# Kernel optimization log

Hardware: AMD Instinct MI355X
Metric: run time of the kernel (lower is better)

Reference implementation:

```python
import jax, jax.numpy as jnp
import numpy as np

N_NODES = 40962
LATENT_DIM = 512
N_EDGES = 655392
NUM_BLOCKS = 4
NUM_HEADS = 4
NUM_FREQ = 32
BASE_PERIOD = 16
NOISE_EMB_DIM = 16
EPS = 1e-5


def setup_inputs() -> dict:
    key = jax.random.key(0)
    ks = jax.random.split(key, 20)
    def w(k, shape, s=0.02):
        return jax.random.normal(k, shape, dtype=jnp.float32) * s
    D, B, C = LATENT_DIM, NUM_BLOCKS, NOISE_EMB_DIM
    z = lambda *s: jnp.zeros(s, jnp.float32)
    return {
        'latent_mesh_nodes': jax.random.normal(ks[0], (N_NODES, D), dtype=jnp.float32),
        'edge_index': jax.random.randint(ks[1], (2, N_EDGES), 0, N_NODES, dtype=jnp.int32),
        'noise_levels': jax.random.uniform(ks[2], (N_NODES, 1), dtype=jnp.float32),
        # Fourier embedding MLP (2F -> C -> C, SiLU)
        'f_w1': w(ks[3], (2 * NUM_FREQ, C)), 'f_b1': z(C),
        'f_w2': w(ks[4], (C, C)), 'f_b2': z(C),
        # per-block conditional LayerNorm 1 (FiLM)
        's1_w': w(ks[5], (B, C, D)), 's1_b': z(B, D),
        'b1_w': w(ks[6], (B, C, D)), 'b1_b': z(B, D),
        # per-block sparse MHA projections
        'wq': w(ks[7], (B, D, D)), 'bq': z(B, D),
        'wk': w(ks[8], (B, D, D)), 'bk': z(B, D),
        'wv': w(ks[9], (B, D, D)), 'bv': z(B, D),
        'wo': w(ks[10], (B, D, D)), 'bo': z(B, D),
        # per-block conditional LayerNorm 2 (FiLM)
        's2_w': w(ks[11], (B, C, D)), 's2_b': z(B, D),
        'b2_w': w(ks[12], (B, C, D)), 'b2_b': z(B, D),
        # per-block feed-forward MLP (D -> D -> D, ReLU)
        'm_w1': w(ks[13], (B, D, D)), 'm_b1': z(B, D),
        'm_w2': w(ks[14], (B, D, D)), 'm_b2': z(B, D),
    }


def _cond_layer_norm(x, cond, sw, sb, bw, bb):
    # LayerNorm without affine params, then FiLM from noise embedding.
    mu = jnp.mean(x, axis=-1, keepdims=True)
    var = jnp.var(x, axis=-1, keepdims=True)
    xn = (x - mu) * jax.lax.rsqrt(var + EPS)
    scale = cond @ sw + sb  # (N, D)
    bias = cond @ bw + bb
    return xn * (1.0 + scale) + bias


def _sparse_attention(x, src, dst, wq, bq, wk, bk, wv, bv, wo, bo):
    N, D = x.shape
    H, Dh = NUM_HEADS, D // NUM_HEADS
    q = ((x @ wq + bq)).reshape(N, H, Dh) * (Dh ** -0.5)
    k = (x @ wk + bk).reshape(N, H, Dh)
    v = (x @ wv + bv).reshape(N, H, Dh)
    # per-edge scores: row (query) = src, col (key) = dst, per head
    scores = jnp.einsum('ehd,ehd->eh', q[src], k[dst])  # (E, H)
    smax = jax.ops.segment_max(scores, src, num_segments=N)  # (N, H)
    ex = jnp.exp(scores - smax[src])
    denom = jax.ops.segment_sum(ex, src, num_segments=N)
    attn = ex / denom[src]  # row-wise sparse softmax
    out = jax.ops.segment_sum(attn[:, :, None] * v[dst], src, num_segments=N)
    return out.reshape(N, D) @ wo + bo


def _forward(x, edge_index, noise_levels, f_w1, f_b1, f_w2, f_b2,
             s1_w, s1_b, b1_w, b1_b, wq, bq, wk, bk, wv, bv, wo, bo,
             s2_w, s2_b, b2_w, b2_b, m_w1, m_b1, m_w2, m_b2):
    src, dst = edge_index[0], edge_index[1]
    # Fourier noise embedding
    freqs = jnp.arange(1, NUM_FREQ + 1, dtype=x.dtype) * (2.0 * np.pi / BASE_PERIOD)
    ph = noise_levels * freqs  # (N, F)
    emb = jnp.concatenate([jnp.sin(ph), jnp.cos(ph)], axis=-1)
    cond = jax.nn.silu(emb @ f_w1 + f_b1) @ f_w2 + f_b2  # (N, C)
    for i in range(NUM_BLOCKS):
        y = _cond_layer_norm(x, cond, s1_w[i], s1_b[i], b1_w[i], b1_b[i])
        y = _sparse_attention(y, src, dst, wq[i], bq[i], wk[i], bk[i],
                              wv[i], bv[i], wo[i], bo[i])
        x = x + y
        y = _cond_layer_norm(x, cond, s2_w[i], s2_b[i], b2_w[i], b2_b[i])
        y = jax.nn.relu(y @ m_w1[i] + m_b1[i]) @ m_w2[i] + m_b2[i]
        x = x + y
    return x


def reference(latent_mesh_nodes, edge_index, noise_levels, f_w1, f_b1, f_w2, f_b2,
              s1_w, s1_b, b1_w, b1_b, wq, bq, wk, bk, wv, bv, wo, bo,
              s2_w, s2_b, b2_w, b2_b, m_w1, m_b1, m_w2, m_b2):
    return _forward(latent_mesh_nodes, edge_index, noise_levels, f_w1, f_b1, f_w2, f_b2,
                    s1_w, s1_b, b1_w, b1_b, wq, bq, wk, bk, wv, bv, wo, bo,
                    s2_w, s2_b, b2_w, b2_b, m_w1, m_b1, m_w2, m_b2)
```

## Files before the change

kernel.cpp:

```cpp
#include <hip/hip_runtime.h>
#include <hip/hip_bf16.h>
#include <stdint.h>

#define N_NODES 40962
#define LATENT  512
#define N_EDGES 655392
#define NFREQ   32
#define NOISE_C 16

typedef unsigned short u16;
typedef unsigned char u8;
typedef __attribute__((ext_vector_type(8))) short short8;
typedef __attribute__((ext_vector_type(4))) float f32x4;
typedef __attribute__((ext_vector_type(2))) float f32x2;

__device__ __forceinline__ float bf2f(u16 u) {
  return __uint_as_float(((uint32_t)u) << 16);
}
__device__ __forceinline__ u16 f2bf(float f) {
  uint32_t u = __float_as_uint(f);
  u += 0x7fffu + ((u >> 16) & 1u);
  return (u16)(u >> 16);
}

__device__ __forceinline__ u8 f2fp8(float f) {
#if __has_builtin(__builtin_amdgcn_cvt_pk_fp8_f32)
  int pk = __builtin_amdgcn_cvt_pk_fp8_f32(f, f, 0, false);
  return (u8)(pk & 0xff);
#else
  uint32_t x = __float_as_uint(f);
  uint32_t s = (x >> 24) & 0x80;
  uint32_t y = x & 0x7fffffff;
  if (__uint_as_float(y) >= 448.f) return (u8)(s | 0x7e);
  y += 0xfffff + ((y >> 20) & 1);
  int e = (int)(y >> 23) - 127 + 7;
  uint32_t m = (y >> 20) & 7;
  if (e < 1) return (u8)s;
  if (e > 15 || (e == 15 && m == 7)) return (u8)(s | 0x7e);
  return (u8)(s | ((uint32_t)e << 3) | m);
#endif
}

__device__ __forceinline__ void fp8x4_to_f32(uint32_t w, float* o) {
#if __has_builtin(__builtin_amdgcn_cvt_pk_f32_fp8)
  f32x2 lo = __builtin_amdgcn_cvt_pk_f32_fp8(w, false);
  f32x2 hi = __builtin_amdgcn_cvt_pk_f32_fp8(w, true);
  o[0] = lo.x; o[1] = lo.y; o[2] = hi.x; o[3] = hi.y;
#else
  #pragma unroll
  for (int i = 0; i < 4; ++i) {
    uint32_t u = (w >> (8 * i)) & 0xff;
    uint32_t e = (u >> 3) & 15, m = u & 7, s = (u & 0x80) << 24;
    o[i] = (e == 0) ? __uint_as_float(s)
                    : __uint_as_float(s | ((e + 120) << 23) | (m << 20));
  }
#endif
}

__global__ void cond_kernel(const float* __restrict__ noise,
                            const float* __restrict__ w1, const float* __restrict__ b1,
                            const float* __restrict__ w2, const float* __restrict__ b2,
                            float* __restrict__ cond)
{
  int n = blockIdx.x * blockDim.x + threadIdx.x;
  if (n >= N_NODES) return;
  float nv = noise[n];
  float emb[2 * NFREQ];
  #pragma unroll
  for (int f = 0; f < NFREQ; ++f) {
    float ph = nv * (0.39269908169872414f * (float)(f + 1));
    emb[f] = __sinf(ph);
    emb[NFREQ + f] = __cosf(ph);
  }
  float h[NOISE_C];
  #pragma unroll
  for (int c = 0; c < NOISE_C; ++c) {
    float a = b1[c];
    for (int j = 0; j < 2 * NFREQ; ++j) a = fmaf(emb[j], w1[j * NOISE_C + c], a);
    h[c] = a * (1.f / (1.f + __expf(-a)));
  }
  #pragma unroll
  for (int c2 = 0; c2 < NOISE_C; ++c2) {
    float a = b2[c2];
    #pragma unroll
    for (int c = 0; c < NOISE_C; ++c) a = fmaf(h[c], w2[c * NOISE_C + c2], a);
    cond[(size_t)n * NOISE_C + c2] = a;
  }
}

__global__ void conv_weights(const float* __restrict__ wq, const float* __restrict__ wk,
                             const float* __restrict__ wv, const float* __restrict__ wo,
                             const float* __restrict__ m1, const float* __restrict__ m2,
                             u16* __restrict__ out)
{
  __shared__ float tile[32][33];
  int z = blockIdx.z;
  int t6 = z >> 2;
  const float* W = (t6 == 0) ? wq : (t6 == 1) ? wk : (t6 == 2) ? wv :
                   (t6 == 3) ? wo : (t6 == 4) ? m1 : m2;
  W += (size_t)(z & 3) * 262144;
  u16* O = out + (size_t)((z & 3) * 6 + t6) * 262144;
  int tx = threadIdx.x, ty = threadIdx.y;
  int j0 = blockIdx.x * 32, k0 = blockIdx.y * 32;
  #pragma unroll
  for (int r = ty; r < 32; r += 8)
    tile[r][tx] = W[(size_t)(k0 + r) * 512 + j0 + tx];
  __syncthreads();
  #pragma unroll
  for (int r = ty; r < 32; r += 8)
    O[(size_t)(j0 + r) * 512 + k0 + tx] = f2bf(tile[tx][r]);
}

__global__ void pack_bias(const float* __restrict__ bq, const float* __restrict__ bk,
                          const float* __restrict__ bv, float* __restrict__ bqkv)
{
  int idx = blockIdx.x * 256 + threadIdx.x;
  if (idx >= 4 * 1536) return;
  int i = idx / 1536, c = idx % 1536;
  float v = (c < 512) ? bq[i * 512 + c] : (c < 1024) ? bk[i * 512 + c - 512]
                                                     : bv[i * 512 + c - 1024];
  bqkv[idx] = v;
}

__global__ void hist_kernel(const int* __restrict__ src, int* __restrict__ deg) {
  int e = blockIdx.x * 256 + threadIdx.x;
  if (e < N_EDGES) atomicAdd(&deg[src[e]], 1);
}

__global__ __launch_bounds__(1024) void scan_kernel(const int* __restrict__ deg,
                                                    int* __restrict__ row_start)
{
  __shared__ int sums[1024];
  int t = threadIdx.x;
  const int chunk = (N_NODES + 1023) / 1024;
  int lo = t * chunk, hi = lo + chunk;
  if (lo > N_NODES) lo = N_NODES;
  if (hi > N_NODES) hi = N_NODES;
  int s = 0;
  for (int i = lo; i < hi; ++i) s += deg[i];
  sums[t] = s;
  __syncthreads();
  for (int off = 1; off < 1024; off <<= 1) {
    int v = (t >= off) ? sums[t - off] : 0;
    __syncthreads();
    sums[t] += v;
    __syncthreads();
  }
  int base = (t > 0) ? sums[t - 1] : 0;
  for (int i = lo; i < hi; ++i) { row_start[i] = base; base += deg[i]; }
  if (t == 1023) row_start[N_NODES] = sums[1023];
}

__global__ void scatter_kernel(const int* __restrict__ src, const int* __restrict__ dst,
                               const int* __restrict__ row_start, int* __restrict__ cursor,
                               int* __restrict__ csr_dst)
{
  int e = blockIdx.x * 256 + threadIdx.x;
  if (e >= N_EDGES) return;
  int s = src[e];
  int p = atomicAdd(&cursor[s], 1);
  csr_dst[row_start[s] + p] = dst[e];
}

__global__ __launch_bounds__(256) void ln_film(
  const float* __restrict__ x, const float* __restrict__ cond,
  const float* __restrict__ sw, const float* __restrict__ sb,
  const float* __restrict__ bw, const float* __restrict__ bb,
  u16* __restrict__ yb)
{
  int n = blockIdx.x;
  int t = threadIdx.x;
  const float* xr = x + (size_t)n * 512;
  float v0 = xr[t], v1 = xr[t + 256];
  float s = v0 + v1, ss = v0 * v0 + v1 * v1;
  #pragma unroll
  for (int o = 32; o > 0; o >>= 1) { s += __shfl_down(s, o); ss += __shfl_down(ss, o); }
  __shared__ float red[8];
  __shared__ float cl[16];
  int wv_ = t >> 6, ln_ = t & 63;
  if (ln_ == 0) { red[wv_] = s; red[4 + wv_] = ss; }
  if (t < 16) cl[t] = cond[(size_t)n * 16 + t];
  __syncthreads();
  s  = red[0] + red[1] + red[2] + red[3];
  ss = red[4] + red[5] + red[6] + red[7];
  float mu = s * (1.f / 512.f);
  float rstd = rsqrtf(ss * (1.f / 512.f) - mu * mu + 1e-5f);
  #pragma unroll
  for (int k = 0; k < 2; ++k) {
    int d = t + k * 256;
    float sc = sb[d], bi = bb[d];
    #pragma unroll
    for (int c = 0; c < 16; ++c) {
      sc = fmaf(cl[c], sw[c * 512 + d], sc);
      bi = fmaf(cl[c], bw[c * 512 + d], bi);
    }
    float xv = k ? v1 : v0;
    yb[(size_t)n * 512 + d] = f2bf((xv - mu) * rstd * (1.f + sc) + bi);
  }
}

template<int MODE, bool RELU, bool RES>
__global__ __launch_bounds__(256) void gemm_bt(
  const u16* __restrict__ A, const u16* __restrict__ Bt,
  const float* __restrict__ bias, const float* __restrict__ res,
  float* __restrict__ Cf, u16* __restrict__ Cb, u8* __restrict__ Cq)
{
  constexpr int M = N_NODES, K = 512;
  __shared__ u16 As[2 * 128 * 32];
  __shared__ u16 Bs[2 * 128 * 32];
  int tid = threadIdx.x;
  int wave = tid >> 6, lane = tid & 63;
  int tn = blockIdx.x * 128, tm = blockIdx.y * 128;
  f32x4 acc[4][4] = {};
  int wm = (wave & 1) * 64, wn = (wave >> 1) * 64;
  int fm = lane & 15, fq = lane >> 4;

  auto stage = [&](int buf, int k0) {
    #pragma unroll
    for (int rr = 0; rr < 2; ++rr) {
      int c = rr * 256 + tid;
      int row = c >> 2, cb = (c & 3) << 3;
      int gr = tm + row; if (gr > M - 1) gr = M - 1;
      __builtin_amdgcn_global_load_lds(
        (const __attribute__((address_space(1))) void*)(uintptr_t)(A + (size_t)gr * K + (k0 + cb)),
        (__attribute__((address_space(3))) void*)(uintptr_t)(As + buf * 4096 + (size_t)(rr * 256 + wave * 64) * 8),
        16, 0, 0);
      int brow = tn + row;
      __builtin_amdgcn_global_load_lds(
        (const __attribute__((address_space(1))) void*)(uintptr_t)(Bt + (size_t)brow * K + (k0 + cb)),
        (__attribute__((address_space(3))) void*)(uintptr_t)(Bs + buf * 4096 + (size_t)(rr * 256 + wave * 64) * 8),
        16, 0, 0);
    }
  };

  stage(0, 0);
  #pragma unroll 4
  for (int it = 0; it < K / 32; ++it) {
    int cur = it & 1;
    __syncthreads();
    if (it + 1 < K / 32) stage(cur ^ 1, (it + 1) * 32);
    const u16* Ab = As + cur * 4096;
    const u16* Bb = Bs + cur * 4096;
    short8 af[4], bf_[4];
    #pragma unroll
    for (int i = 0; i < 4; ++i) {
      af[i]  = *(const short8*)(Ab + (wm + i * 16 + fm) * 32 + fq * 8);
      bf_[i] = *(const short8*)(Bb + (wn + i * 16 + fm) * 32 + fq * 8);
    }
    #pragma unroll
    for (int mi = 0; mi < 4; ++mi)
      #pragma unroll
      for (int ni = 0; ni < 4; ++ni)
        acc[mi][ni] = __builtin_amdgcn_mfma_f32_16x16x32_bf16(af[mi], bf_[ni], acc[mi][ni], 0, 0, 0);
  }

  #pragma unroll
  for (int mi = 0; mi < 4; ++mi) {
    #pragma unroll
    for (int ni = 0; ni < 4; ++ni) {
      int col = tn + wn + ni * 16 + fm;
      float bvv = bias[col];
      int rowb = tm + wm + mi * 16 + fq * 4;
      #pragma unroll
      for (int r = 0; r < 4; ++r) {
        int gr = rowb + r;
        if (gr < M) {
          float v = acc[mi][ni][r] + bvv;
          if (RELU) v = fmaxf(v, 0.f);
          if (RES)  v += res[(size_t)gr * 512 + col];
          if (MODE == 0) {
            Cf[(size_t)gr * 512 + col] = v;
          } else if (MODE == 1) {
            Cb[(size_t)gr * 512 + col] = f2bf(v);
          } else {
            u8* row_p = Cq + (size_t)gr * 2048;
            if (col < 512) *(u16*)(row_p + 2 * col) = f2bf(v);
            else           row_p[512 + col] = f2fp8(v);
          }
        }
      }
    }
  }
}

__global__ __launch_bounds__(256) void attn_kernel(
  const u8* __restrict__ qkv,
  const int* __restrict__ row_start, const int* __restrict__ csr_dst,
  u16* __restrict__ ab)
{
  int wave = threadIdx.x >> 6, lane = threadIdx.x & 63;
  int n = blockIdx.x * 4 + wave;
  if (n >= N_NODES) return;
  float qf[8];
  {
    short8 q8 = *(const short8*)(qkv + (size_t)n * 2048 + lane * 16);
    #pragma unroll
    for (int j = 0; j < 8; ++j) qf[j] = bf2f((u16)q8[j]);
  }
  float m = -1e30f, l = 0.f;
  float acc[8];
  #pragma unroll
  for (int j = 0; j < 8; ++j) acc[j] = 0.f;
  int e0 = row_start[n], e1 = row_start[n + 1];
  int deg = e1 - e0;
  if (deg > 0) {
    int koff = 1024 + lane * 8, voff = 1536 + lane * 8;
    int d0 = csr_dst[e0];
    int d1 = (deg > 1) ? csr_dst[e0 + 1] : d0;
    uint2 ku0 = *(const uint2*)(qkv + (size_t)d0 * 2048 + koff);
    uint2 vu0 = *(const uint2*)(qkv + (size_t)d0 * 2048 + voff);
    uint2 ku1 = *(const uint2*)(qkv + (size_t)d1 * 2048 + koff);
    uint2 vu1 = *(const uint2*)(qkv + (size_t)d1 * 2048 + voff);
    for (int t = 0; t < deg; t += 2) {
      int p0 = e0 + t + 2, p1 = e0 + t + 3;
      int dn0 = (p0 < e1) ? csr_dst[p0] : d0;
      int dn1 = (p1 < e1) ? csr_dst[p1] : d0;
      uint2 kn0 = *(const uint2*)(qkv + (size_t)dn0 * 2048 + koff);
      uint2 vn0 = *(const uint2*)(qkv + (size_t)dn0 * 2048 + voff);
      uint2 kn1 = *(const uint2*)(qkv + (size_t)dn1 * 2048 + koff);
      uint2 vn1 = *(const uint2*)(qkv + (size_t)dn1 * 2048 + voff);
      float k0f[8], k1f[8];
      fp8x4_to_f32(ku0.x, k0f); fp8x4_to_f32(ku0.y, k0f + 4);
      fp8x4_to_f32(ku1.x, k1f); fp8x4_to_f32(ku1.y, k1f + 4);
      float s0 = 0.f, s1 = 0.f;
      #pragma unroll
      for (int j = 0; j < 8; ++j) { s0 = fmaf(qf[j], k0f[j], s0); s1 = fmaf(qf[j], k1f[j], s1); }
      s0 += __shfl_xor(s0, 1); s1 += __shfl_xor(s1, 1);
      s0 += __shfl_xor(s0, 2); s1 += __shfl_xor(s1, 2);
      s0 += __shfl_xor(s0, 4); s1 += __shfl_xor(s1, 4);
      s0 += __shfl_xor(s0, 8); s1 += __shfl_xor(s1, 8);
      s0 *= 0.088388347648318447f;
      s1 = (t + 1 < deg) ? s1 * 0.088388347648318447f : -1e30f;
      float mx = fmaxf(m, fmaxf(s0, s1));
      float al = __expf(m - mx);
      float pp0 = __expf(s0 - mx);
      float pp1 = __expf(s1 - mx);
      l = l * al + pp0 + pp1;
      float v0f[8], v1f[8];
      fp8x4_to_f32(vu0.x, v0f); fp8x4_to_f32(vu0.y, v0f + 4);
      fp8x4_to_f32(vu1.x, v1f); fp8x4_to_f32(vu1.y, v1f + 4);
      #pragma unroll
      for (int j = 0; j < 8; ++j)
        acc[j] = fmaf(acc[j], al, fmaf(pp0, v0f[j], pp1 * v1f[j]));
      m = mx;
      ku0 = kn0; vu0 = vn0; ku1 = kn1; vu1 = vn1;
    }
  }
  float rl = (l > 0.f) ? 1.f / l : 0.f;
  short8 o8;
  #pragma unroll
  for (int j = 0; j < 8; ++j) o8[j] = (short)f2bf(acc[j] * rl);
  *(short8*)(ab + (size_t)n * 512 + lane * 8) = o8;
}

extern "C" void kernel_launch(void* const* d_in, const int* in_sizes, int n_in,
                              void* d_out, int out_size, void* d_ws, size_t ws_size,
                              hipStream_t stream)
{
  const float* x0    = (const float*)d_in[0];
  const int*   edge  = (const int*)d_in[1];
  const float* noise = (const float*)d_in[2];
  const float* f_w1  = (const float*)d_in[3];
  const float* f_b1  = (const float*)d_in[4];
  const float* f_w2  = (const float*)d_in[5];
  const float* f_b2  = (const float*)d_in[6];
  const float* s1_w  = (const float*)d_in[7];
  const float* s1_b  = (const float*)d_in[8];
  const float* b1_w  = (const float*)d_in[9];
  const float* b1_b  = (const float*)d_in[10];
  const float* wq    = (const float*)d_in[11];
  const float* bq    = (const float*)d_in[12];
  const float* wk    = (const float*)d_in[13];
  const float* bk    = (const float*)d_in[14];
  const float* wv    = (const float*)d_in[15];
  const float* bv    = (const float*)d_in[16];
  const float* wo    = (const float*)d_in[17];
  const float* bo    = (const float*)d_in[18];
  const float* s2_w  = (const float*)d_in[19];
  const float* s2_b  = (const float*)d_in[20];
  const float* b2_w  = (const float*)d_in[21];
  const float* b2_b  = (const float*)d_in[22];
  const float* m_w1  = (const float*)d_in[23];
  const float* m_b1  = (const float*)d_in[24];
  const float* m_w2  = (const float*)d_in[25];
  const float* m_b2  = (const float*)d_in[26];
  float* xout = (float*)d_out;

  char* w = (char*)d_ws;
  auto alloc = [&](size_t bytes) -> char* {
    char* p = w; w += (bytes + 255) & ~(size_t)255; return p;
  };
  u16*  Wt     = (u16*)alloc(24ull * 512 * 512 * 2);
  float* cond  = (float*)alloc((size_t)N_NODES * 16 * 4);
  float* bqkv  = (float*)alloc(4 * 1536 * 4);
  u16*  ybf    = (u16*)alloc((size_t)N_NODES * 512 * 2);
  u16*  hbf    = (u16*)alloc((size_t)N_NODES * 512 * 2);
  u8*   qkvb   = (u8*)alloc((size_t)N_NODES * 2048);
  int*  deg    = (int*)alloc((size_t)N_NODES * 4);
  int*  cursor = (int*)alloc((size_t)N_NODES * 4);
  int*  rowst  = (int*)alloc((size_t)(N_NODES + 1) * 4);
  int*  csrd   = (int*)alloc((size_t)N_EDGES * 4);

  conv_weights<<<dim3(16, 16, 24), dim3(32, 8), 0, stream>>>(wq, wk, wv, wo, m_w1, m_w2, Wt);
  cond_kernel<<<(N_NODES + 255) / 256, 256, 0, stream>>>(noise, f_w1, f_b1, f_w2, f_b2, cond);
  pack_bias<<<(4 * 1536 + 255) / 256, 256, 0, stream>>>(bq, bk, bv, bqkv);
  hipMemsetAsync(deg, 0, (size_t)N_NODES * 4, stream);
  hipMemsetAsync(cursor, 0, (size_t)N_NODES * 4, stream);
  const int* src = edge;
  const int* dst = edge + N_EDGES;
  hist_kernel<<<(N_EDGES + 255) / 256, 256, 0, stream>>>(src, deg);
  scan_kernel<<<1, 1024, 0, stream>>>(deg, rowst);
  scatter_kernel<<<(N_EDGES + 255) / 256, 256, 0, stream>>>(src, dst, rowst, cursor, csrd);

  dim3 g_qkv(12, 321), g_512(4, 321);
  const float* xin = x0;
  for (int i = 0; i < 4; ++i) {
    const u16* Wb = Wt + (size_t)i * 6 * 262144;
    ln_film<<<N_NODES, 256, 0, stream>>>(xin, cond, s1_w + i * 8192, s1_b + i * 512,
                                         b1_w + i * 8192, b1_b + i * 512, ybf);
    gemm_bt<2, false, false><<<g_qkv, 256, 0, stream>>>(ybf, Wb, bqkv + i * 1536,
                                                        nullptr, nullptr, nullptr, qkvb);
    attn_kernel<<<(N_NODES + 3) / 4, 256, 0, stream>>>(qkvb, rowst, csrd, ybf);
    gemm_bt<0, false, true><<<g_512, 256, 0, stream>>>(ybf, Wb + 3 * 262144,
                                                       bo + i * 512, xin, xout, nullptr, nullptr);
    ln_film<<<N_NODES, 256, 0, stream>>>(xout, cond, s2_w + i * 8192, s2_b + i * 512,
                                         b2_w + i * 8192, b2_b + i * 512, ybf);
    gemm_bt<1, true, false><<<g_512, 256, 0, stream>>>(ybf, Wb + 4 * 262144,
                                                       m_b1 + i * 512, nullptr, nullptr, hbf, nullptr);
    gemm_bt<0, false, true><<<g_512, 256, 0, stream>>>(hbf, Wb + 5 * 262144,
                                                       m_b2 + i * 512, xout, xout, nullptr, nullptr);
    xin = xout;
  }
}
```

Before: 3.160 ms.

## Add 256x256-tile pipelined QKV GEMM and XCD-aware workgroup remapping

Result: faster. 3.058 ms (-3.2%).

```diff
diff --git a/kernel.cpp b/kernel.cpp
--- a/kernel.cpp
+++ b/kernel.cpp
@@ -57,6 +57,12 @@
 #endif
 }
 
+__device__ __forceinline__ int xcd_remap(int id, int nwg) {
+  int q = nwg >> 3, r = nwg & 7;
+  int xc = id & 7, jj = id >> 3;
+  return (xc < r ? xc * (q + 1) : r * (q + 1) + (xc - r) * q) + jj;
+}
+
 __global__ void cond_kernel(const float* __restrict__ noise,
                             const float* __restrict__ w1, const float* __restrict__ b1,
                             const float* __restrict__ w2, const float* __restrict__ b2,
@@ -199,18 +205,137 @@
   }
 }
 
+__global__ __launch_bounds__(512, 2) void gemm256_qkv(
+  const u16* __restrict__ A, const u16* __restrict__ Bt,
+  const float* __restrict__ bias, u8* __restrict__ Cq)
+{
+  constexpr int M = N_NODES;
+  constexpr int NBX = 6;
+  constexpr int NT = 8;
+  __shared__ u16 As[2][256 * 64];
+  __shared__ u16 Bs[2][256 * 64];
+  int tid = threadIdx.x;
+  int wid = tid >> 6, lane = tid & 63;
+  int wm = wid >> 2, wn = wid & 3;
+  int fm = lane & 15, fq = lane >> 4;
+  int l3 = lane >> 3, l7 = lane & 7;
+  int swz16 = (l7 ^ l3) * 8;
+
+  int wg = xcd_remap(blockIdx.x, gridDim.x);
+  int tn = (wg % NBX) * 256;
+  int tm = (wg / NBX) * 256;
+
+  f32x4 acc[8][4] = {};
+
+  auto stage_half = [&](u16* ldsmat, const u16* __restrict__ G, int rowbase,
+                        int h, int t, bool clampM) {
+    #pragma unroll
+    for (int rr = 0; rr < 2; ++rr) {
+      int rowblk = h * 128 + (wid * 2 + rr) * 8;
+      int grow = rowbase + rowblk + l3;
+      if (clampM && grow > M - 1) grow = M - 1;
+      const u16* src = G + (size_t)grow * 512 + t * 64 + swz16;
+      u16* dstb = ldsmat + rowblk * 64;
+      __builtin_amdgcn_global_load_lds(
+        (const __attribute__((address_space(1))) void*)(uintptr_t)src,
+        (__attribute__((address_space(3))) void*)(uintptr_t)dstb, 16, 0, 0);
+    }
+  };
+
+  auto phase = [&](int d, int qm, int qn) {
+    const u16* Ab = &As[d][0];
+    const u16* Bb = &Bs[d][0];
+    short8 a4[4][2], b2[2][2];
+    #pragma unroll
+    for (int i = 0; i < 4; ++i) {
+      int ar = wm * 128 + qm * 64 + i * 16 + fm;
+      #pragma unroll
+      for (int ks = 0; ks < 2; ++ks)
+        a4[i][ks] = *(const short8*)(Ab + ar * 64 + ((ks * 32 + fq * 8) ^ ((fm & 7) * 8)));
+    }
+    #pragma unroll
+    for (int j = 0; j < 2; ++j) {
+      int bc = wn * 64 + qn * 32 + j * 16 + fm;
+      #pragma unroll
+      for (int ks = 0; ks < 2; ++ks)
+        b2[j][ks] = *(const short8*)(Bb + bc * 64 + ((ks * 32 + fq * 8) ^ ((fm & 7) * 8)));
+    }
+    __builtin_amdgcn_s_setprio(1);
+    #pragma unroll
+    for (int i = 0; i < 4; ++i)
+      #pragma unroll
+      for (int j = 0; j < 2; ++j)
+        #pragma unroll
+        for (int ks = 0; ks < 2; ++ks)
+          acc[qm * 4 + i][qn * 2 + j] = __builtin_amdgcn_mfma_f32_16x16x32_bf16(
+              a4[i][ks], b2[j][ks], acc[qm * 4 + i][qn * 2 + j], 0, 0, 0);
+    __builtin_amdgcn_s_setprio(0);
+    __builtin_amdgcn_s_barrier();
+    __builtin_amdgcn_sched_barrier(0);
+  };
+
+  stage_half(As[0], A, tm, 0, 0, true);
+  stage_half(As[0], A, tm, 1, 0, true);
+  stage_half(Bs[0], Bt, tn, 0, 0, false);
+  stage_half(Bs[0], Bt, tn, 1, 0, false);
+
+  #pragma unroll 2
+  for (int t = 0; t < NT; ++t) {
+    int d = t & 1;
+    if (t + 1 < NT) {
+      stage_half(As[d ^ 1], A, tm, 0, t + 1, true);
+      stage_half(Bs[d ^ 1], Bt, tn, 0, t + 1, false);
+      asm volatile("s_waitcnt vmcnt(4)" ::: "memory");
+    } else {
+      asm volatile("s_waitcnt vmcnt(0)" ::: "memory");
+    }
+    __builtin_amdgcn_sched_barrier(0);
+    __builtin_amdgcn_s_barrier();
+    __builtin_amdgcn_sched_barrier(0);
+    phase(d, 0, 0);
+    phase(d, 1, 0);
+    if (t + 1 < NT) {
+      stage_half(As[d ^ 1], A, tm, 1, t + 1, true);
+      stage_half(Bs[d ^ 1], Bt, tn, 1, t + 1, false);
+    }
+    phase(d, 0, 1);
+    phase(d, 1, 1);
+  }
+
+  #pragma unroll
+  for (int i = 0; i < 8; ++i) {
+    int rowb = tm + wm * 128 + i * 16 + fq * 4;
+    #pragma unroll
+    for (int j = 0; j < 4; ++j) {
+      int col = tn + wn * 64 + j * 16 + fm;
+      float bvv = bias[col];
+      #pragma unroll
+      for (int r = 0; r < 4; ++r) {
+        int gr = rowb + r;
+        if (gr < M) {
+          float v = acc[i][j][r] + bvv;
+          u8* row_p = Cq + (size_t)gr * 2048;
+          if (col < 512) *(u16*)(row_p + 2 * col) = f2bf(v);
+          else           row_p[512 + col] = f2fp8(v);
+        }
+      }
+    }
+  }
+}
+
 template<int MODE, bool RELU, bool RES>
 __global__ __launch_bounds__(256) void gemm_bt(
   const u16* __restrict__ A, const u16* __restrict__ Bt,
   const float* __restrict__ bias, const float* __restrict__ res,
-  float* __restrict__ Cf, u16* __restrict__ Cb, u8* __restrict__ Cq)
+  float* __restrict__ Cf, u16* __restrict__ Cb, int nbx)
 {
   constexpr int M = N_NODES, K = 512;
   __shared__ u16 As[2 * 128 * 32];
   __shared__ u16 Bs[2 * 128 * 32];
   int tid = threadIdx.x;
   int wave = tid >> 6, lane = tid & 63;
-  int tn = blockIdx.x * 128, tm = blockIdx.y * 128;
+  int wg = xcd_remap(blockIdx.x, gridDim.x);
+  int tn = (wg % nbx) * 128, tm = (wg / nbx) * 128;
   f32x4 acc[4][4] = {};
   int wm = (wave & 1) * 64, wn = (wave >> 1) * 64;
   int fm = lane & 15, fq = lane >> 4;
@@ -268,15 +393,8 @@
           float v = acc[mi][ni][r] + bvv;
           if (RELU) v = fmaxf(v, 0.f);
           if (RES)  v += res[(size_t)gr * 512 + col];
-          if (MODE == 0) {
-            Cf[(size_t)gr * 512 + col] = v;
-          } else if (MODE == 1) {
-            Cb[(size_t)gr * 512 + col] = f2bf(v);
-          } else {
-            u8* row_p = Cq + (size_t)gr * 2048;
-            if (col < 512) *(u16*)(row_p + 2 * col) = f2bf(v);
-            else           row_p[512 + col] = f2fp8(v);
-          }
+          if (MODE == 0) Cf[(size_t)gr * 512 + col] = v;
+          else           Cb[(size_t)gr * 512 + col] = f2bf(v);
         }
       }
     }
@@ -412,23 +530,23 @@
   scan_kernel<<<1, 1024, 0, stream>>>(deg, rowst);
   scatter_kernel<<<(N_EDGES + 255) / 256, 256, 0, stream>>>(src, dst, rowst, cursor, csrd);
 
-  dim3 g_qkv(12, 321), g_512(4, 321);
+  const int g_qkv = 6 * ((N_NODES + 255) / 256);
+  const int g_512 = 4 * ((N_NODES + 127) / 128);
   const float* xin = x0;
   for (int i = 0; i < 4; ++i) {
     const u16* Wb = Wt + (size_t)i * 6 * 262144;
     ln_film<<<N_NODES, 256, 0, stream>>>(xin, cond, s1_w + i * 8192, s1_b + i * 512,
                                          b1_w + i * 8192, b1_b + i * 512, ybf);
-    gemm_bt<2, false, false><<<g_qkv, 256, 0, stream>>>(ybf, Wb, bqkv + i * 1536,
-                                                        nullptr, nullptr, nullptr, qkvb);
+    gemm256_qkv<<<g_qkv, 512, 0, stream>>>(ybf, Wb, bqkv + i * 1536, qkvb);
     attn_kernel<<<(N_NODES + 3) / 4, 256, 0, stream>>>(qkvb, rowst, csrd, ybf);
     gemm_bt<0, false, true><<<g_512, 256, 0, stream>>>(ybf, Wb + 3 * 262144,
-                                                       bo + i * 512, xin, xout, nullptr, nullptr);
+                                                       bo + i * 512, xin, xout, nullptr, 4);
     ln_film<<<N_NODES, 256, 0, stream>>>(xout, cond, s2_w + i * 8192, s2_b + i * 512,
                                          b2_w + i * 8192, b2_b + i * 512, ybf);
     gemm_bt<1, true, false><<<g_512, 256, 0, stream>>>(ybf, Wb + 4 * 262144,
-                                                       m_b1 + i * 512, nullptr, nullptr, hbf, nullptr);
+                                                       m_b1 + i * 512, nullptr, nullptr, hbf, 4);
     gemm_bt<0, false, true><<<g_512, 256, 0, stream>>>(hbf, Wb + 5 * 262144,
-                                                       m_b2 + i * 512, xout, xout, nullptr, nullptr);
+                                                       m_b2 + i * 512, xout, xout, nullptr, 4);
     xin = xout;
   }
 }
```
